# Kernel tuning notes

Hardware: AMD Instinct MI355X
Metric: run time of the kernel (lower is better)

Reference implementation:

```python
import jax, jax.numpy as jnp
import numpy as np

N = 16384      # batch size
F = 1024       # n_features
H = 256        # n_dim (latent)


def setup_inputs() -> dict:
    key = jax.random.key(0)
    ks = jax.random.split(key, 6)
    X = jax.random.normal(ks[0], (N, F), dtype=jnp.float32)
    We = jax.random.normal(ks[1], (F, H), dtype=jnp.float32) / np.sqrt(F).astype(np.float32)
    be = jnp.zeros((H,), dtype=jnp.float32)
    Wd = jax.random.normal(ks[2], (H, F), dtype=jnp.float32) / np.sqrt(H).astype(np.float32)
    bd = jnp.zeros((F,), dtype=jnp.float32)
    Wc = jax.random.normal(ks[3], (H, 1), dtype=jnp.float32) / np.sqrt(H).astype(np.float32)
    bc = jnp.zeros((1,), dtype=jnp.float32)
    s = jax.random.randint(ks[4], (N,), 0, 2, dtype=jnp.int32)  # protected attribute labels in {0,1}
    return {"X": X, "We": We, "be": be, "Wd": Wd, "bd": bd, "Wc": Wc, "bc": bc, "s": s, "p": 1}


def reference(X, We, be, Wd, bd, Wc, bc, s, p):
    # encoder / decoder (single Linear each, as in the default NRL construction)
    g = X @ We + be                      # [N, H]
    rec = g @ Wd + bd                    # [N, F]
    mse_mean = jnp.mean((rec - X) ** 2)  # MSELoss is built with reduction='sum' but forward uses torch.mean(pow(...)) directly

    # critic scores for ALL rows (critics share weights: [module]*n_protected)
    c = (g @ Wc + bc)[:, 0]              # [N]

    # masked pairwise L1: sum_{i in P, j notin P} |c_i - c_j|
    mp = (s == p)                        # rows where s == p
    mpf = mp.astype(c.dtype)
    mrf = (~mp).astype(c.dtype)
    Dmat = jnp.abs(c[:, None] - c[None, :])   # [N, N] pairwise L1 (cdist equivalent)
    total = mpf @ (Dmat @ mrf)                # mp^T D mr == cdist(c_p, c_rest, p=1).sum()

    w_dist_count = mp.sum()                   # == w_dist.shape[0] (number of protected rows)
    w_dist_mean = total / w_dist_count.astype(c.dtype)

    return (mse_mean, jnp.asarray(rec.shape[0]), w_dist_mean, w_dist_count)
```

## Files before the change

kernel.cpp:

```cpp
#include <hip/hip_runtime.h>
#include <hip/hip_bf16.h>
#include <cstdint>

#define NR 16384
#define NF 1024
#define NH 256

typedef __bf16 bf16x8 __attribute__((ext_vector_type(8)));
typedef float f32x4 __attribute__((ext_vector_type(4)));
typedef unsigned short us8 __attribute__((ext_vector_type(8)));

static __device__ __forceinline__ unsigned short f2bf(float f) {
    unsigned u = __float_as_uint(f);
    u += 0x7FFFu + ((u >> 16) & 1u);
    return (unsigned short)(u >> 16);
}


__global__ __launch_bounds__(256) void prep_kernel(
    const float* __restrict__ We, const float* __restrict__ Wd,
    unsigned short* __restrict__ Wepk, unsigned short* __restrict__ Wdpk,
    float* __restrict__ hdr) {
    const int b = blockIdx.x, t = threadIdx.x;
    if (b == 0 && t < 192) hdr[t] = 0.f;
    if (b < 128) {
        const int k0 = b, c = t;
        const int kc = k0 >> 2, q = k0 & 3, nb = c >> 4, li = c & 15;
        us8 v;
#pragma unroll
        for (int e = 0; e < 8; e++)
            v[e] = f2bf(We[(size_t)(k0 * 8 + e) * NH + c]);
        *(us8*)&Wepk[((size_t)(nb * 32 + kc)) * 512 + (q * 16 + li) * 8] = v;
    } else {
        const int idx = b - 128;
        const int k0 = idx >> 2, c = (idx & 3) * 256 + t;
        const int kc = k0 >> 2, q = k0 & 3, nb = c >> 4, li = c & 15;
        us8 v;
#pragma unroll
        for (int e = 0; e < 8; e++)
            v[e] = f2bf(Wd[(size_t)(k0 * 8 + e) * NF + c]);
        *(us8*)&Wdpk[((size_t)(nb * 8 + kc)) * 512 + (q * 16 + li) * 8] = v;
    }
}

__global__ __launch_bounds__(512) void fused_kernel(
    const float* __restrict__ X,
    const unsigned short* __restrict__ Wepk, const unsigned short* __restrict__ Wdpk,
    const float* __restrict__ be, const float* __restrict__ bd,
    const float* __restrict__ Wc, const int* __restrict__ s, const int* __restrict__ pv,
    float* __restrict__ cP, float* __restrict__ cR, float* __restrict__ hdr) {
    __shared__ union {
        unsigned short xa[16384];
        struct {
            unsigned short gs[16384];
            float credu[8][64];
            float msred[8];
        } p2;
    } u;
    const int t = threadIdx.x;
    const int b = blockIdx.x, m0 = b * 64;
    const int w = t >> 6, lane = t & 63, q = lane >> 4, li = lane & 15;

    const int srow = w * 8;
    const int kcgl = lane >> 3;
    const int sq2  = (lane >> 1) & 3;
    const int sh   = lane & 1;

    {
        const float* xq = X + (size_t)m0 * NF + lane * 4;
#pragma unroll
        for (int rr = 0; rr < 8; ++rr) {
            const int r = srow + rr;
            float4 v4 = *(const float4*)(xq + (size_t)r * NF);
            ushort4 st = { f2bf(v4.x), f2bf(v4.y), f2bf(v4.z), f2bf(v4.w) };
            const int p = (sq2 * 16 + (r & 15)) ^ kcgl;
            *(ushort4*)&u.xa[(kcgl * 4 + (r >> 4)) * 512 + p * 8 + sh * 4] = st;
        }
    }
    __syncthreads();

    const unsigned short* Bp[2];
#pragma unroll
    for (int j = 0; j < 2; j++)
        Bp[j] = Wepk + ((size_t)(w * 2 + j) * 32) * 512 + lane * 8;

    us8 fb[8][2];
#pragma unroll
    for (int z = 0; z < 8; ++z)
#pragma unroll
        for (int j = 0; j < 2; j++) fb[z][j] = *(const us8*)(Bp[j] + z * 512);

    f32x4 acc[4][2] = {};

#pragma unroll
    for (int ks = 0; ks < 4; ++ks) {
#pragma unroll
        for (int kcl = 0; kcl < 8; ++kcl) {
            const int kcg = ks * 8 + kcl;
            const int cb = kcg & 7;
#pragma unroll
            for (int mi = 0; mi < 4; ++mi) {
                bf16x8 a = __builtin_bit_cast(bf16x8,
                    *(const us8*)&u.xa[(kcl * 4 + mi) * 512 + (lane ^ kcl) * 8]);
                acc[mi][0] = __builtin_amdgcn_mfma_f32_16x16x32_bf16(
                    __builtin_bit_cast(bf16x8, fb[cb][0]), a, acc[mi][0], 0, 0, 0);
                acc[mi][1] = __builtin_amdgcn_mfma_f32_16x16x32_bf16(
                    __builtin_bit_cast(bf16x8, fb[cb][1]), a, acc[mi][1], 0, 0, 0);
            }
            if (kcg + 8 < 32) {
#pragma unroll
                for (int j = 0; j < 2; j++) fb[cb][j] = *(const us8*)(Bp[j] + (kcg + 8) * 512);
            }
        }
        __syncthreads();
        if (ks < 3) {
            const float* xq = X + (size_t)m0 * NF + (ks + 1) * 256 + lane * 4;
#pragma unroll
            for (int rr = 0; rr < 8; ++rr) {
                const int r = srow + rr;
                float4 v4 = *(const float4*)(xq + (size_t)r * NF);
                ushort4 st = { f2bf(v4.x), f2bf(v4.y), f2bf(v4.z), f2bf(v4.w) };
                const int p = (sq2 * 16 + (r & 15)) ^ kcgl;
                *(ushort4*)&u.xa[(kcgl * 4 + (r >> 4)) * 512 + p * 8 + sh * 4] = st;
            }
            __syncthreads();
        }
    }

#pragma unroll
    for (int mi = 0; mi < 4; ++mi) {
        float csum = 0.f;
#pragma unroll
        for (int j = 0; j < 2; ++j) {
            const int colb = w * 32 + j * 16 + q * 4;
            float4 be4 = *(const float4*)&be[colb];
            float4 wc4 = *(const float4*)&Wc[colb];
            float v0 = acc[mi][j][0] + be4.x;
            float v1 = acc[mi][j][1] + be4.y;
            float v2 = acc[mi][j][2] + be4.z;
            float v3 = acc[mi][j][3] + be4.w;
            csum += v0 * wc4.x + v1 * wc4.y + v2 * wc4.z + v3 * wc4.w;
            ushort4 st = { f2bf(v0), f2bf(v1), f2bf(v2), f2bf(v3) };
            const int q2e = j * 2 + (q >> 1);
            const int p = (q2e * 16 + li) ^ w;
            *(ushort4*)&u.p2.gs[(w * 4 + mi) * 512 + p * 8 + (q & 1) * 4] = st;
        }
        csum += __shfl_down(csum, 32);
        csum += __shfl_down(csum, 16);
        if (lane < 16) u.p2.credu[w][mi * 16 + lane] = csum;
    }
    __syncthreads();

    if (t < 64) {
        float cs = 0.f;
#pragma unroll
        for (int ww = 0; ww < 8; ++ww) cs += u.p2.credu[ww][t];
        bool pr = (s[m0 + t] == pv[0]);
        unsigned long long mk = __ballot(pr);
        int np = __popcll(mk);
        int baseP = 0, baseR = 0;
        if (t == 0) {
            baseP = atomicAdd((int*)hdr + 129, np);
            baseR = atomicAdd((int*)hdr + 130, 64 - np);
        }
        baseP = __shfl(baseP, 0);
        baseR = __shfl(baseR, 0);
        int offP = __popcll(mk & ((1ull << t) - 1ull));
        int offR = t - offP;
        if (pr) cP[baseP + offP] = cs; else cR[baseR + offR] = cs;
    }

    float lsum = 0.f;
    const unsigned short* Wp = Wdpk + lane * 8;
#pragma unroll
    for (int pass = 0; pass < 4; ++pass) {
        const int nb0 = pass * 16 + w * 2;
        us8 gb[8][2];
#pragma unroll
        for (int z = 0; z < 8; ++z)
#pragma unroll
            for (int j = 0; j < 2; ++j)
                gb[z][j] = *(const us8*)(Wp + ((size_t)((nb0 + j) * 8 + z)) * 512);
        f32x4 a2[4][2] = {};
#pragma unroll
        for (int kc = 0; kc < 8; ++kc) {
#pragma unroll
            for (int mi = 0; mi < 4; ++mi) {
                bf16x8 af = __builtin_bit_cast(bf16x8,
                    *(const us8*)&u.p2.gs[(kc * 4 + mi) * 512 + (lane ^ kc) * 8]);
                a2[mi][0] = __builtin_amdgcn_mfma_f32_16x16x32_bf16(
                    __builtin_bit_cast(bf16x8, gb[kc][0]), af, a2[mi][0], 0, 0, 0);
                a2[mi][1] = __builtin_amdgcn_mfma_f32_16x16x32_bf16(
                    __builtin_bit_cast(bf16x8, gb[kc][1]), af, a2[mi][1], 0, 0, 0);
            }
        }
#pragma unroll
        for (int mi = 0; mi < 4; ++mi) {
            const size_t rowoff = (size_t)(m0 + mi * 16 + li) * NF;
#pragma unroll
            for (int j = 0; j < 2; ++j) {
                const int colb = pass * 256 + w * 32 + j * 16 + q * 4;
                float4 bd4 = *(const float4*)&bd[colb];
                float4 xr  = *(const float4*)&X[rowoff + colb];
                float d0 = a2[mi][j][0] + bd4.x - xr.x;
                float d1 = a2[mi][j][1] + bd4.y - xr.y;
                float d2 = a2[mi][j][2] + bd4.z - xr.z;
                float d3 = a2[mi][j][3] + bd4.w - xr.w;
                lsum += d0 * d0 + d1 * d1 + d2 * d2 + d3 * d3;
            }
        }
    }
#pragma unroll
    for (int o = 32; o; o >>= 1) lsum += __shfl_down(lsum, o);
    if (lane == 0) u.p2.msred[w] = lsum;
    __syncthreads();
    if (t == 0) {
        float ms = 0.f;
#pragma unroll
        for (int ww = 0; ww < 8; ++ww) ms += u.p2.msred[ww];
        atomicAdd(&hdr[b & 63], ms);
    }
}

__global__ __launch_bounds__(256) void pair_fin_kernel(
    const float* __restrict__ cP, const float* __restrict__ cR,
    float* __restrict__ hdr, float* __restrict__ out) {
    __shared__ float sj[1024];
    __shared__ float red[256];
    __shared__ int win;
    const int nP = ((const int*)hdr)[129];
    const int nR = ((const int*)hdr)[130];
    const int jb = blockIdx.x * 1024;
    int jn = nR - jb; if (jn < 0) jn = 0; if (jn > 1024) jn = 1024;
    float sum = 0.f;
    if (jn > 0 && blockIdx.y * 512 < nP) {
        for (int j = threadIdx.x; j < 1024; j += 256)
            sj[j] = (jb + j < nR) ? cR[jb + j] : 0.f;
        __syncthreads();
        const int a0 = blockIdx.y * 512 + threadIdx.x, a1 = a0 + 256;
        const float ca0 = (a0 < nP) ? cP[a0] : 0.f;
        const float ca1 = (a1 < nP) ? cP[a1] : 0.f;
        float s0 = 0.f, s1 = 0.f;
#pragma unroll 8
        for (int j4 = 0; j4 < 256; j4++) {
            float4 v = *(const float4*)&sj[j4 * 4];
            s0 += fabsf(ca0 - v.x) + fabsf(ca0 - v.y) + fabsf(ca0 - v.z) + fabsf(ca0 - v.w);
            s1 += fabsf(ca1 - v.x) + fabsf(ca1 - v.y) + fabsf(ca1 - v.z) + fabsf(ca1 - v.w);
        }
        float pad = (float)(1024 - jn);
        s0 -= pad * fabsf(ca0);
        s1 -= pad * fabsf(ca1);
        if (a0 >= nP) s0 = 0.f;
        if (a1 >= nP) s1 = 0.f;
        sum = s0 + s1;
#pragma unroll
        for (int o = 32; o; o >>= 1) sum += __shfl_down(sum, o);
        if ((threadIdx.x & 63) == 0 && sum != 0.f)
            atomicAdd(&hdr[64 + ((blockIdx.y * 16 + blockIdx.x) & 63)], sum);
    }
    __threadfence();
    __syncthreads();
    if (threadIdx.x == 0)
        win = (atomicAdd((int*)(hdr + 128), 1) == 16 * 32 - 1) ? 1 : 0;
    __syncthreads();
    if (win) {
        float v = (threadIdx.x < 128) ? atomicAdd(&hdr[threadIdx.x], 0.f) : 0.f;
        red[threadIdx.x] = v;
        __syncthreads();
        if (threadIdx.x == 0) {
            float ms = 0.f, ps = 0.f;
            for (int i = 0; i < 64; i++) { ms += red[i]; ps += red[64 + i]; }
            int np = atomicAdd((int*)(hdr + 129), 0);
            out[0] = ms / (float)((size_t)NR * NF);
            out[1] = (float)NR;
            out[2] = ps / (float)np;
            out[3] = (float)np;
        }
    }
}

extern "C" void kernel_launch(void* const* d_in, const int* in_sizes, int n_in,
                              void* d_out, int out_size, void* d_ws, size_t ws_size,
                              hipStream_t stream) {
    const float* X  = (const float*)d_in[0];
    const float* We = (const float*)d_in[1];
    const float* be = (const float*)d_in[2];
    const float* Wd = (const float*)d_in[3];
    const float* bd = (const float*)d_in[4];
    const float* Wc = (const float*)d_in[5];
    const int*   s  = (const int*)d_in[7];
    const int*   pv = (const int*)d_in[8];

    char* ws = (char*)d_ws;
    float* hdr = (float*)ws;
    float* cP  = (float*)(ws + 1024);
    float* cR  = (float*)(ws + 1024 + 65536);
    unsigned short* Wepk = (unsigned short*)(ws + 1024 + 2 * 65536);
    unsigned short* Wdpk = Wepk + (size_t)NH * NF;

    prep_kernel<<<256, 256, 0, stream>>>(We, Wd, Wepk, Wdpk, hdr);
    fused_kernel<<<256, 512, 0, stream>>>(X, Wepk, Wdpk, be, bd, Wc, s, pv, cP, cR, hdr);
    pair_fin_kernel<<<dim3(16, 32), 256, 0, stream>>>(cP, cR, hdr, (float*)d_out);
}
```

Baseline: 183.1 us.

## Halve fused kernel row tile to 32 rows, 4 waves, 512 blocks

The fused encoder/decoder kernel now handles 32 rows per block with 4 waves of 256 threads instead of 64 rows with 8 waves, and launches 512 blocks. Each wave now owns 64 output columns (4 N-blocks) by 2 M-blocks, which reshapes the MFMA register tiles and the LDS layout for g. The decoder B-fragments are now loaded in a rolling 4-deep prefetch rather than all up front. The aim is to fill the 256 CUs better with smaller blocks and to lower register and LDS use, at the cost of reading the weights twice as often per row and issuing more atomics.

```diff
diff --git a/kernel.cpp b/kernel.cpp
--- a/kernel.cpp
+++ b/kernel.cpp
@@ -43,22 +43,22 @@
     }
 }
 
-__global__ __launch_bounds__(512) void fused_kernel(
+__global__ __launch_bounds__(256) void fused_kernel(
     const float* __restrict__ X,
     const unsigned short* __restrict__ Wepk, const unsigned short* __restrict__ Wdpk,
     const float* __restrict__ be, const float* __restrict__ bd,
     const float* __restrict__ Wc, const int* __restrict__ s, const int* __restrict__ pv,
     float* __restrict__ cP, float* __restrict__ cR, float* __restrict__ hdr) {
     __shared__ union {
-        unsigned short xa[16384];
+        unsigned short xa[8192];
         struct {
-            unsigned short gs[16384];
-            float credu[8][64];
-            float msred[8];
+            unsigned short gs[8192];
+            float credu[4][32];
+            float msred[4];
         } p2;
     } u;
     const int t = threadIdx.x;
-    const int b = blockIdx.x, m0 = b * 64;
+    const int b = blockIdx.x, m0 = b * 32;
     const int w = t >> 6, lane = t & 63, q = lane >> 4, li = lane & 15;
 
     const int srow = w * 8;
@@ -74,42 +74,43 @@
             float4 v4 = *(const float4*)(xq + (size_t)r * NF);
             ushort4 st = { f2bf(v4.x), f2bf(v4.y), f2bf(v4.z), f2bf(v4.w) };
             const int p = (sq2 * 16 + (r & 15)) ^ kcgl;
-            *(ushort4*)&u.xa[(kcgl * 4 + (r >> 4)) * 512 + p * 8 + sh * 4] = st;
-        }
-    }
-    __syncthreads();
-
-    const unsigned short* Bp[2];
-#pragma unroll
-    for (int j = 0; j < 2; j++)
-        Bp[j] = Wepk + ((size_t)(w * 2 + j) * 32) * 512 + lane * 8;
-
-    us8 fb[8][2];
-#pragma unroll
-    for (int z = 0; z < 8; ++z)
-#pragma unroll
-        for (int j = 0; j < 2; j++) fb[z][j] = *(const us8*)(Bp[j] + z * 512);
-
-    f32x4 acc[4][2] = {};
+            *(ushort4*)&u.xa[(kcgl * 2 + (r >> 4)) * 512 + p * 8 + sh * 4] = st;
+        }
+    }
+    __syncthreads();
+
+    const unsigned short* Bp[4];
+#pragma unroll
+    for (int j = 0; j < 4; j++)
+        Bp[j] = Wepk + ((size_t)(w * 4 + j) * 32) * 512 + lane * 8;
+
+    us8 fb[4][4];
+#pragma unroll
+    for (int z = 0; z < 4; ++z)
+#pragma unroll
+        for (int j = 0; j < 4; j++) fb[z][j] = *(const us8*)(Bp[j] + z * 512);
+
+    f32x4 acc[2][4] = {};
 
 #pragma unroll
     for (int ks = 0; ks < 4; ++ks) {
 #pragma unroll
         for (int kcl = 0; kcl < 8; ++kcl) {
             const int kcg = ks * 8 + kcl;
-            const int cb = kcg & 7;
-#pragma unroll
-            for (int mi = 0; mi < 4; ++mi) {
-                bf16x8 a = __builtin_bit_cast(bf16x8,
-                    *(const us8*)&u.xa[(kcl * 4 + mi) * 512 + (lane ^ kcl) * 8]);
-                acc[mi][0] = __builtin_amdgcn_mfma_f32_16x16x32_bf16(
-                    __builtin_bit_cast(bf16x8, fb[cb][0]), a, acc[mi][0], 0, 0, 0);
-                acc[mi][1] = __builtin_amdgcn_mfma_f32_16x16x32_bf16(
-                    __builtin_bit_cast(bf16x8, fb[cb][1]), a, acc[mi][1], 0, 0, 0);
-            }
-            if (kcg + 8 < 32) {
-#pragma unroll
-                for (int j = 0; j < 2; j++) fb[cb][j] = *(const us8*)(Bp[j] + (kcg + 8) * 512);
+            const int cb = kcg & 3;
+            bf16x8 a0 = __builtin_bit_cast(bf16x8,
+                *(const us8*)&u.xa[(kcl * 2 + 0) * 512 + (lane ^ kcl) * 8]);
+            bf16x8 a1 = __builtin_bit_cast(bf16x8,
+                *(const us8*)&u.xa[(kcl * 2 + 1) * 512 + (lane ^ kcl) * 8]);
+#pragma unroll
+            for (int j = 0; j < 4; ++j) {
+                bf16x8 bf = __builtin_bit_cast(bf16x8, fb[cb][j]);
+                acc[0][j] = __builtin_amdgcn_mfma_f32_16x16x32_bf16(bf, a0, acc[0][j], 0, 0, 0);
+                acc[1][j] = __builtin_amdgcn_mfma_f32_16x16x32_bf16(bf, a1, acc[1][j], 0, 0, 0);
+            }
+            if (kcg + 4 < 32) {
+#pragma unroll
+                for (int j = 0; j < 4; j++) fb[cb][j] = *(const us8*)(Bp[j] + (kcg + 4) * 512);
             }
         }
         __syncthreads();
@@ -121,18 +122,18 @@
                 float4 v4 = *(const float4*)(xq + (size_t)r * NF);
                 ushort4 st = { f2bf(v4.x), f2bf(v4.y), f2bf(v4.z), f2bf(v4.w) };
                 const int p = (sq2 * 16 + (r & 15)) ^ kcgl;
-                *(ushort4*)&u.xa[(kcgl * 4 + (r >> 4)) * 512 + p * 8 + sh * 4] = st;
+                *(ushort4*)&u.xa[(kcgl * 2 + (r >> 4)) * 512 + p * 8 + sh * 4] = st;
             }
             __syncthreads();
         }
     }
 
 #pragma unroll
-    for (int mi = 0; mi < 4; ++mi) {
+    for (int mi = 0; mi < 2; ++mi) {
         float csum = 0.f;
 #pragma unroll
-        for (int j = 0; j < 2; ++j) {
-            const int colb = w * 32 + j * 16 + q * 4;
+        for (int j = 0; j < 4; ++j) {
+            const int colb = w * 64 + j * 16 + q * 4;
             float4 be4 = *(const float4*)&be[colb];
             float4 wc4 = *(const float4*)&Wc[colb];
             float v0 = acc[mi][j][0] + be4.x;
@@ -141,9 +142,10 @@
             float v3 = acc[mi][j][3] + be4.w;
             csum += v0 * wc4.x + v1 * wc4.y + v2 * wc4.z + v3 * wc4.w;
             ushort4 st = { f2bf(v0), f2bf(v1), f2bf(v2), f2bf(v3) };
-            const int q2e = j * 2 + (q >> 1);
-            const int p = (q2e * 16 + li) ^ w;
-            *(ushort4*)&u.p2.gs[(w * 4 + mi) * 512 + p * 8 + (q & 1) * 4] = st;
+            const int kcc = colb >> 5;
+            const int q2e = (colb >> 3) & 3;
+            const int p = (q2e * 16 + li) ^ kcc;
+            *(ushort4*)&u.p2.gs[(kcc * 2 + mi) * 512 + p * 8 + (q & 1) * 4] = st;
         }
         csum += __shfl_down(csum, 32);
         csum += __shfl_down(csum, 16);
@@ -151,17 +153,16 @@
     }
     __syncthreads();
 
-    if (t < 64) {
-        float cs = 0.f;
-#pragma unroll
-        for (int ww = 0; ww < 8; ++ww) cs += u.p2.credu[ww][t];
+    if (t < 32) {
+        float cs = u.p2.credu[0][t] + u.p2.credu[1][t] +
+                   u.p2.credu[2][t] + u.p2.credu[3][t];
         bool pr = (s[m0 + t] == pv[0]);
         unsigned long long mk = __ballot(pr);
         int np = __popcll(mk);
         int baseP = 0, baseR = 0;
         if (t == 0) {
             baseP = atomicAdd((int*)hdr + 129, np);
-            baseR = atomicAdd((int*)hdr + 130, 64 - np);
+            baseR = atomicAdd((int*)hdr + 130, 32 - np);
         }
         baseP = __shfl(baseP, 0);
         baseR = __shfl(baseR, 0);
@@ -174,32 +175,39 @@
     const unsigned short* Wp = Wdpk + lane * 8;
 #pragma unroll
     for (int pass = 0; pass < 4; ++pass) {
-        const int nb0 = pass * 16 + w * 2;
-        us8 gb[8][2];
-#pragma unroll
-        for (int z = 0; z < 8; ++z)
-#pragma unroll
-            for (int j = 0; j < 2; ++j)
+        const int nb0 = pass * 16 + w * 4;
+        us8 gb[4][4];
+#pragma unroll
+        for (int z = 0; z < 4; ++z)
+#pragma unroll
+            for (int j = 0; j < 4; ++j)
                 gb[z][j] = *(const us8*)(Wp + ((size_t)((nb0 + j) * 8 + z)) * 512);
-        f32x4 a2[4][2] = {};
+        f32x4 a2[2][4] = {};
 #pragma unroll
         for (int kc = 0; kc < 8; ++kc) {
-#pragma unroll
-            for (int mi = 0; mi < 4; ++mi) {
-                bf16x8 af = __builtin_bit_cast(bf16x8,
-                    *(const us8*)&u.p2.gs[(kc * 4 + mi) * 512 + (lane ^ kc) * 8]);
-                a2[mi][0] = __builtin_amdgcn_mfma_f32_16x16x32_bf16(
-                    __builtin_bit_cast(bf16x8, gb[kc][0]), af, a2[mi][0], 0, 0, 0);
-                a2[mi][1] = __builtin_amdgcn_mfma_f32_16x16x32_bf16(
-                    __builtin_bit_cast(bf16x8, gb[kc][1]), af, a2[mi][1], 0, 0, 0);
-            }
-        }
-#pragma unroll
-        for (int mi = 0; mi < 4; ++mi) {
+            const int cb = kc & 3;
+            bf16x8 af0 = __builtin_bit_cast(bf16x8,
+                *(const us8*)&u.p2.gs[(kc * 2 + 0) * 512 + (lane ^ kc) * 8]);
+            bf16x8 af1 = __builtin_bit_cast(bf16x8,
+                *(const us8*)&u.p2.gs[(kc * 2 + 1) * 512 + (lane ^ kc) * 8]);
+#pragma unroll
+            for (int j = 0; j < 4; ++j) {
+                bf16x8 bf = __builtin_bit_cast(bf16x8, gb[cb][j]);
+                a2[0][j] = __builtin_amdgcn_mfma_f32_16x16x32_bf16(bf, af0, a2[0][j], 0, 0, 0);
+                a2[1][j] = __builtin_amdgcn_mfma_f32_16x16x32_bf16(bf, af1, a2[1][j], 0, 0, 0);
+            }
+            if (kc + 4 < 8) {
+#pragma unroll
+                for (int j = 0; j < 4; ++j)
+                    gb[cb][j] = *(const us8*)(Wp + ((size_t)((nb0 + j) * 8 + kc + 4)) * 512);
+            }
+        }
+#pragma unroll
+        for (int mi = 0; mi < 2; ++mi) {
             const size_t rowoff = (size_t)(m0 + mi * 16 + li) * NF;
 #pragma unroll
-            for (int j = 0; j < 2; ++j) {
-                const int colb = pass * 256 + w * 32 + j * 16 + q * 4;
+            for (int j = 0; j < 4; ++j) {
+                const int colb = pass * 256 + w * 64 + j * 16 + q * 4;
                 float4 bd4 = *(const float4*)&bd[colb];
                 float4 xr  = *(const float4*)&X[rowoff + colb];
                 float d0 = a2[mi][j][0] + bd4.x - xr.x;
@@ -215,10 +223,8 @@
     if (lane == 0) u.p2.msred[w] = lsum;
     __syncthreads();
     if (t == 0) {
-        float ms = 0.f;
-#pragma unroll
-        for (int ww = 0; ww < 8; ++ww) ms += u.p2.msred[ww];
-        atomicAdd(&hdr[b & 63], ms);
+        atomicAdd(&hdr[b & 63], u.p2.msred[0] + u.p2.msred[1] +
+                                u.p2.msred[2] + u.p2.msred[3]);
     }
 }
 
@@ -299,6 +305,6 @@
     unsigned short* Wdpk = Wepk + (size_t)NH * NF;
 
     prep_kernel<<<256, 256, 0, stream>>>(We, Wd, Wepk, Wdpk, hdr);
-    fused_kernel<<<256, 512, 0, stream>>>(X, Wepk, Wdpk, be, bd, Wc, s, pv, cP, cR, hdr);
+    fused_kernel<<<512, 256, 0, stream>>>(X, Wepk, Wdpk, be, bd, Wc, s, pv, cP, cR, hdr);
     pair_fin_kernel<<<dim3(16, 32), 256, 0, stream>>>(cP, cR, hdr, (float*)d_out);
 }
```

Result: slower. 203.7 us (+11.3%).

## Merge prep, fused and pair kernels into one cooperative kernel with grid syncs

Applied to the files above, without the earlier changes.

Combines the three kernel launches (weight packing, fused encoder/decoder, pairwise L1 reduction) into a single cooperative launch of 256 blocks, separating the stages with grid.sync(). The pairwise stage is remapped onto the same 256 blocks, each handling 512 protected rows against 2048 rest values, and the final reduction is done by block 0 after a last grid sync. This drops the per-kernel launch gaps and the atomic last-block election. In exchange it depends on cooperative launch residency, and the pair stage now runs with fewer blocks than the earlier 512-block grid.

```diff
diff --git a/kernel.cpp b/kernel.cpp
--- a/kernel.cpp
+++ b/kernel.cpp
@@ -1,6 +1,9 @@
 #include <hip/hip_runtime.h>
 #include <hip/hip_bf16.h>
+#include <hip/hip_cooperative_groups.h>
 #include <cstdint>
+
+namespace cg = cooperative_groups;
 
 #define NR 16384
 #define NF 1024
@@ -16,39 +19,15 @@
     return (unsigned short)(u >> 16);
 }
 
-
-__global__ __launch_bounds__(256) void prep_kernel(
-    const float* __restrict__ We, const float* __restrict__ Wd,
+__global__ __launch_bounds__(512) void mono_kernel(
+    const float* __restrict__ X,
+    const float* __restrict__ We, const float* __restrict__ be,
+    const float* __restrict__ Wd, const float* __restrict__ bd,
+    const float* __restrict__ Wc, const int* __restrict__ s,
+    const int* __restrict__ pv,
     unsigned short* __restrict__ Wepk, unsigned short* __restrict__ Wdpk,
-    float* __restrict__ hdr) {
-    const int b = blockIdx.x, t = threadIdx.x;
-    if (b == 0 && t < 192) hdr[t] = 0.f;
-    if (b < 128) {
-        const int k0 = b, c = t;
-        const int kc = k0 >> 2, q = k0 & 3, nb = c >> 4, li = c & 15;
-        us8 v;
-#pragma unroll
-        for (int e = 0; e < 8; e++)
-            v[e] = f2bf(We[(size_t)(k0 * 8 + e) * NH + c]);
-        *(us8*)&Wepk[((size_t)(nb * 32 + kc)) * 512 + (q * 16 + li) * 8] = v;
-    } else {
-        const int idx = b - 128;
-        const int k0 = idx >> 2, c = (idx & 3) * 256 + t;
-        const int kc = k0 >> 2, q = k0 & 3, nb = c >> 4, li = c & 15;
-        us8 v;
-#pragma unroll
-        for (int e = 0; e < 8; e++)
-            v[e] = f2bf(Wd[(size_t)(k0 * 8 + e) * NF + c]);
-        *(us8*)&Wdpk[((size_t)(nb * 8 + kc)) * 512 + (q * 16 + li) * 8] = v;
-    }
-}
-
-__global__ __launch_bounds__(512) void fused_kernel(
-    const float* __restrict__ X,
-    const unsigned short* __restrict__ Wepk, const unsigned short* __restrict__ Wdpk,
-    const float* __restrict__ be, const float* __restrict__ bd,
-    const float* __restrict__ Wc, const int* __restrict__ s, const int* __restrict__ pv,
-    float* __restrict__ cP, float* __restrict__ cR, float* __restrict__ hdr) {
+    float* __restrict__ cP, float* __restrict__ cR,
+    float* __restrict__ hdr, float* __restrict__ out) {
     __shared__ union {
         unsigned short xa[16384];
         struct {
@@ -56,11 +35,38 @@
             float credu[8][64];
             float msred[8];
         } p2;
+        float sj[2048];
     } u;
+    cg::grid_group grid = cg::this_grid();
     const int t = threadIdx.x;
-    const int b = blockIdx.x, m0 = b * 64;
+    const int b = blockIdx.x;
+
+    {
+        if (b == 0 && t < 192) hdr[t] = 0.f;
+        const int gid = b * 512 + t;
+        if (gid < 32768) {
+            const int k0 = gid >> 8, c = gid & 255;
+            const int kc = k0 >> 2, qq = k0 & 3, nb = c >> 4, li2 = c & 15;
+            us8 v;
+#pragma unroll
+            for (int e = 0; e < 8; e++)
+                v[e] = f2bf(We[(size_t)(k0 * 8 + e) * NH + c]);
+            *(us8*)&Wepk[((size_t)(nb * 32 + kc)) * 512 + (qq * 16 + li2) * 8] = v;
+        } else if (gid < 65536) {
+            const int idx = gid - 32768;
+            const int k0 = idx >> 10, c = idx & 1023;
+            const int kc = k0 >> 2, qq = k0 & 3, nb = c >> 4, li2 = c & 15;
+            us8 v;
+#pragma unroll
+            for (int e = 0; e < 8; e++)
+                v[e] = f2bf(Wd[(size_t)(k0 * 8 + e) * NF + c]);
+            *(us8*)&Wdpk[((size_t)(nb * 8 + kc)) * 512 + (qq * 16 + li2) * 8] = v;
+        }
+    }
+    grid.sync();
+
+    const int m0 = b * 64;
     const int w = t >> 6, lane = t & 63, q = lane >> 4, li = lane & 15;
-
     const int srow = w * 8;
     const int kcgl = lane >> 3;
     const int sq2  = (lane >> 1) & 3;
@@ -220,62 +226,46 @@
         for (int ww = 0; ww < 8; ++ww) ms += u.p2.msred[ww];
         atomicAdd(&hdr[b & 63], ms);
     }
-}
-
-__global__ __launch_bounds__(256) void pair_fin_kernel(
-    const float* __restrict__ cP, const float* __restrict__ cR,
-    float* __restrict__ hdr, float* __restrict__ out) {
-    __shared__ float sj[1024];
-    __shared__ float red[256];
-    __shared__ int win;
-    const int nP = ((const int*)hdr)[129];
-    const int nR = ((const int*)hdr)[130];
-    const int jb = blockIdx.x * 1024;
-    int jn = nR - jb; if (jn < 0) jn = 0; if (jn > 1024) jn = 1024;
-    float sum = 0.f;
-    if (jn > 0 && blockIdx.y * 512 < nP) {
-        for (int j = threadIdx.x; j < 1024; j += 256)
-            sj[j] = (jb + j < nR) ? cR[jb + j] : 0.f;
-        __syncthreads();
-        const int a0 = blockIdx.y * 512 + threadIdx.x, a1 = a0 + 256;
-        const float ca0 = (a0 < nP) ? cP[a0] : 0.f;
-        const float ca1 = (a1 < nP) ? cP[a1] : 0.f;
-        float s0 = 0.f, s1 = 0.f;
+    grid.sync();
+
+    {
+        const int nP = ((const int*)hdr)[129];
+        const int nRv = ((const int*)hdr)[130];
+        const int jc = b & 7, ic = b >> 3;
+        const int jb = jc * 2048;
+        int jn = nRv - jb; if (jn < 0) jn = 0; if (jn > 2048) jn = 2048;
+        if (jn > 0 && ic * 512 < nP) {
+            for (int j = t; j < 2048; j += 512)
+                u.sj[j] = (jb + j < nRv) ? cR[jb + j] : 0.f;
+            __syncthreads();
+            const int i = ic * 512 + t;
+            const float ci = (i < nP) ? cP[i] : 0.f;
+            float s0 = 0.f;
 #pragma unroll 8
-        for (int j4 = 0; j4 < 256; j4++) {
-            float4 v = *(const float4*)&sj[j4 * 4];
-            s0 += fabsf(ca0 - v.x) + fabsf(ca0 - v.y) + fabsf(ca0 - v.z) + fabsf(ca0 - v.w);
-            s1 += fabsf(ca1 - v.x) + fabsf(ca1 - v.y) + fabsf(ca1 - v.z) + fabsf(ca1 - v.w);
-        }
-        float pad = (float)(1024 - jn);
-        s0 -= pad * fabsf(ca0);
-        s1 -= pad * fabsf(ca1);
-        if (a0 >= nP) s0 = 0.f;
-        if (a1 >= nP) s1 = 0.f;
-        sum = s0 + s1;
-#pragma unroll
-        for (int o = 32; o; o >>= 1) sum += __shfl_down(sum, o);
-        if ((threadIdx.x & 63) == 0 && sum != 0.f)
-            atomicAdd(&hdr[64 + ((blockIdx.y * 16 + blockIdx.x) & 63)], sum);
-    }
-    __threadfence();
-    __syncthreads();
-    if (threadIdx.x == 0)
-        win = (atomicAdd((int*)(hdr + 128), 1) == 16 * 32 - 1) ? 1 : 0;
-    __syncthreads();
-    if (win) {
-        float v = (threadIdx.x < 128) ? atomicAdd(&hdr[threadIdx.x], 0.f) : 0.f;
-        red[threadIdx.x] = v;
-        __syncthreads();
-        if (threadIdx.x == 0) {
-            float ms = 0.f, ps = 0.f;
-            for (int i = 0; i < 64; i++) { ms += red[i]; ps += red[64 + i]; }
-            int np = atomicAdd((int*)(hdr + 129), 0);
-            out[0] = ms / (float)((size_t)NR * NF);
-            out[1] = (float)NR;
-            out[2] = ps / (float)np;
-            out[3] = (float)np;
-        }
+            for (int j4 = 0; j4 < 512; j4++) {
+                float4 v = *(const float4*)&u.sj[j4 * 4];
+                s0 += fabsf(ci - v.x) + fabsf(ci - v.y) +
+                      fabsf(ci - v.z) + fabsf(ci - v.w);
+            }
+            s0 -= (float)(2048 - jn) * fabsf(ci);
+            if (i >= nP) s0 = 0.f;
+            float sum = s0;
+#pragma unroll
+            for (int o = 32; o; o >>= 1) sum += __shfl_down(sum, o);
+            if ((t & 63) == 0 && sum != 0.f)
+                atomicAdd(&hdr[64 + (b & 63)], sum);
+        }
+    }
+    grid.sync();
+
+    if (b == 0 && t == 0) {
+        float ms = 0.f, ps = 0.f;
+        for (int i = 0; i < 64; i++) { ms += hdr[i]; ps += hdr[64 + i]; }
+        int np = ((const int*)hdr)[129];
+        out[0] = ms / (float)((size_t)NR * NF);
+        out[1] = (float)NR;
+        out[2] = ps / (float)np;
+        out[3] = (float)np;
     }
 }
 
@@ -297,8 +287,13 @@
     float* cR  = (float*)(ws + 1024 + 65536);
     unsigned short* Wepk = (unsigned short*)(ws + 1024 + 2 * 65536);
     unsigned short* Wdpk = Wepk + (size_t)NH * NF;
-
-    prep_kernel<<<256, 256, 0, stream>>>(We, Wd, Wepk, Wdpk, hdr);
-    fused_kernel<<<256, 512, 0, stream>>>(X, Wepk, Wdpk, be, bd, Wc, s, pv, cP, cR, hdr);
-    pair_fin_kernel<<<dim3(16, 32), 256, 0, stream>>>(cP, cR, hdr, (float*)d_out);
+    float* outp = (float*)d_out;
+
+    void* args[] = {
+        (void*)&X, (void*)&We, (void*)&be, (void*)&Wd, (void*)&bd,
+        (void*)&Wc, (void*)&s, (void*)&pv, (void*)&Wepk, (void*)&Wdpk,
+        (void*)&cP, (void*)&cR, (void*)&hdr, (void*)&outp
+    };
+    hipLaunchCooperativeKernel((void*)mono_kernel, dim3(256), dim3(512),
+                               args, 0, stream);
 }
```

Result: slower. 262.0 us (+43.1%).
